# Optimization experiments

Measured on AMD Instinct MI355X. Metric: run time of the kernel, lower is better.

Reference implementation:

```python
import jax, jax.numpy as jnp
import numpy as np

N = 10000          # num_nodes
E_DIR = 160000     # directed random edges before symmetrization
B = 8              # batch
IN = 64            # input_size per node
UNITS = 64         # num_units
K = 2              # max_diffusion_step -> num_matrices = K + 1
LAMBDA_MAX = 1.5   # stand-in for eigsh largest-eigenvalue estimate


def _build_scaled_laplacian():
    # L_scaled = (2/lambda_max) * (I - D^-1/2 A D^-1/2) - I, as sparse COO
    rng = np.random.default_rng(0)
    src = rng.integers(0, N, E_DIR)
    dst = rng.integers(0, N, E_DIR)
    # symmetrize A = max(A, A^T) by duplicating edges both ways
    r = np.concatenate([src, dst])
    c = np.concatenate([dst, src])
    w = np.ones(2 * E_DIR, np.float32)
    deg = np.zeros(N, np.float32)
    np.add.at(deg, r, w)
    d_inv_sqrt = np.where(deg > 0, deg ** -0.5, 0.0).astype(np.float32)
    coef = np.float32(2.0 / LAMBDA_MAX)
    off_vals = (-coef * d_inv_sqrt[r] * d_inv_sqrt[c] * w).astype(np.float32)
    diag_idx = np.arange(N, dtype=np.int32)
    diag_vals = np.full(N, coef - 1.0, np.float32)
    rows = np.concatenate([r.astype(np.int32), diag_idx])
    cols = np.concatenate([c.astype(np.int32), diag_idx])
    vals = np.concatenate([off_vals, diag_vals])
    return rows, cols, vals  # nnz = 2*E_DIR + N = 330000


def setup_inputs() -> dict:
    key = jax.random.key(0)
    k_in, k_w = jax.random.split(key)
    rows, cols, vals = _build_scaled_laplacian()
    num_matrices = K + 1
    fan_in = IN * num_matrices
    xavier = np.sqrt(6.0 / (fan_in + UNITS)).astype(np.float32)
    return {
        "inputs": jax.random.normal(k_in, (B, N * IN), dtype=jnp.float32),
        "rows": jnp.asarray(rows),
        "cols": jnp.asarray(cols),
        "vals": jnp.asarray(vals),
        "weights": jax.random.uniform(k_w, (fan_in, UNITS), dtype=jnp.float32,
                                      minval=-xavier, maxval=xavier),
        "biases": jnp.zeros((UNITS,), dtype=jnp.float32),
    }


def reference(inputs, rows, cols, vals, weights, biases):
    batch = inputs.shape[0]
    x = inputs.reshape(batch, N, -1)              # [B, N, in]
    in_size = x.shape[2]
    # x0: [N, in*B]
    x0 = jnp.transpose(x, (1, 2, 0)).reshape(N, in_size * batch)

    def spmm(h):  # sparse Laplacian @ dense
        return jax.ops.segment_sum(vals[:, None] * h[cols], rows, num_segments=N)

    # Chebyshev recursion: T0 = x0, T1 = L x0, Tk = 2 L Tk-1 - Tk-2
    xs = [x0]
    x1 = spmm(x0)
    xs.append(x1)
    xk_1, xk_2 = x1, x0
    for _ in range(2, K + 1):
        x2 = 2.0 * spmm(xk_1) - xk_2
        xs.append(x2)
        xk_1, xk_2 = x2, xk_1

    num_matrices = K + 1
    xcat = jnp.stack(xs, axis=0)                              # [M, N, in*B]
    xcat = xcat.reshape(num_matrices, N, in_size, batch)      # [M, N, in, B]
    xcat = jnp.transpose(xcat, (3, 1, 2, 0))                  # [B, N, in, M]
    xcat = xcat.reshape(batch * N, in_size * num_matrices)
    out = xcat @ weights + biases
    return out.reshape(batch, N, UNITS)
```

## Files before the change

kernel.cpp:

```cpp
#include <hip/hip_runtime.h>
#include <hip/hip_fp16.h>

#define N_NODES 10000
#define BATCH   8
#define IN_SZ   64
#define UNITS   64
#define ROW_U   256
#define RCAP    96
#define STR     (N_NODES * 64)

typedef unsigned int uint;
typedef unsigned short ushort;
typedef __attribute__((ext_vector_type(8))) _Float16 half8;
typedef __attribute__((ext_vector_type(4))) float float4v;
typedef __attribute__((ext_vector_type(4))) uint uint4v;
typedef __attribute__((ext_vector_type(2))) uint uint2v;

__device__ inline uint f2bf_bits(float f) {
    uint u = __float_as_uint(f);
    uint r = ((u >> 16) & 1u) + 0x7FFFu;
    return (u + r) >> 16;
}
__device__ inline uint pack2h(float a, float b) {
    return (uint)__half_as_ushort(__float2half(a)) |
           ((uint)__half_as_ushort(__float2half(b)) << 16);
}
__device__ inline float h_lo(uint u) {
    return __half2float(__ushort_as_half((ushort)(u & 0xFFFFu)));
}
__device__ inline float h_hi(uint u) {
    return __half2float(__ushort_as_half((ushort)(u >> 16)));
}


__global__ __launch_bounds__(256) void k_transpose_scatter(
    const float4v* __restrict__ in4, uint* __restrict__ x0,
    const int* __restrict__ rows, const int* __restrict__ cols,
    const float* __restrict__ vals, uint* __restrict__ cursor,
    uint* __restrict__ edges, const float* __restrict__ W,
    ushort* __restrict__ wt, int nnz) {
    int gid = blockIdx.x * 256 + threadIdx.x;
    uint V = cursor[N_NODES];
    if (gid < nnz) {
        int  r   = rows[gid];
        uint pos = atomicAdd(&cursor[r], 1u) - V;
        edges[r * RCAP + pos] = (uint)cols[gid] | (f2bf_bits(vals[gid]) << 16);
    }
    if (gid < 192 * 64) {
        int u   = gid / 192;
        int col = gid - u * 192;
        int m   = col >> 6, i = col & 63;
        wt[gid] = (ushort)__half_as_ushort(__float2half(W[(i * 3 + m) * 64 + u]));
    }
    int i4 = gid & 15;
    int b  = (gid >> 4) & 7;
    int n  = gid >> 7;
    float4v v = __builtin_nontemporal_load(
        &in4[((size_t)b * N_NODES + n) * 16 + i4]);
    int c_u = b * 32 + i4 * 2;
    int q   = c_u >> 6;
    uint2v pk;
    pk.x = pack2h(v.x, v.y);
    pk.y = pack2h(v.z, v.w);
    *(uint2v*)(x0 + (size_t)q * STR + (size_t)n * 64 + (c_u & 63)) = pk;
}

#define READE(EP, KB)                                                         \
    {                                                                         \
        uint _es = ((KB) < 8) ? erec : erec2;                                 \
        int  _i0 = (((KB) * 8) & 63);                                         \
        _Pragma("unroll") for (int jj = 0; jj < 8; ++jj)                      \
            EP[jj] = __builtin_amdgcn_readlane(_es, _i0 + jj);                \
    }

#define GATHERX(XR, EP)                                                       \
    _Pragma("unroll") for (int jj = 0; jj < 8; ++jj) {                        \
        uint c = EP[jj] & 0x3FFFu;                                            \
        if (c > N_NODES - 1) c = N_NODES - 1;      \
        XR[jj] = xq[c * 64u + lane];             \
    }

#define FMA8(EP, XR)                                                          \
    _Pragma("unroll") for (int jj = 0; jj < 8; ++jj) {                        \
        float vj = __uint_as_float(EP[jj] & 0xFFFF0000u);    \
        a0 += vj * h_lo(XR[jj]);                           \
        a1 += vj * h_hi(XR[jj]);                           \
    }

__global__ __launch_bounds__(256) void k_spmm(const uint* __restrict__ cursor,
                                              const uint* __restrict__ edges,
                                              const uint* __restrict__ xin,
                                              uint* __restrict__ xout,
                                              const uint* __restrict__ xsub,
                                              float scale) {
    int L    = blockIdx.x;
    int q    = (L & 7) >> 1;
    int rb   = ((L >> 3) << 1) | (L & 1);
    int wave = threadIdx.x >> 6;
    uint lane = threadIdx.x & 63;
    int row  = rb * 4 + wave;

    const uint* xq = xin + (size_t)q * STR;
    int base = row * RCAP;
    uint V   = cursor[N_NODES];
    int cnt  = (int)__builtin_amdgcn_readfirstlane(cursor[row] - V);
    int nblk = (cnt + 7) >> 3;

    uint erec = edges[base + (int)lane];
    if ((int)lane >= cnt) erec &= 0x3FFFu;
    uint erec2 = 0;
    if (cnt > 64) {
        erec2 = edges[base + 64 + (int)lane];
        if ((int)lane + 64 >= cnt) erec2 &= 0x3FFFu;
    }

    uint sx = 0;
    if (xsub) sx = xsub[(size_t)q * STR + (size_t)row * 64 + lane];

    float a0 = 0.f, a1 = 0.f;
    uint epA[8], epB[8], xA[8], xB[8];
    READE(epA, 0);
    GATHERX(xA, epA);
    int k = 0;
    for (; k + 2 <= nblk; k += 2) {
        READE(epB, k + 1);
        GATHERX(xB, epB);
        FMA8(epA, xA);
        if (k + 2 < nblk) {
            READE(epA, k + 2);
            GATHERX(xA, epA);
        }
        FMA8(epB, xB);
    }
    if (k < nblk) FMA8(epA, xA);

    float o0 = scale * a0, o1 = scale * a1;
    if (xsub) {
        o0 -= h_lo(sx);
        o1 -= h_hi(sx);
    }
    xout[(size_t)q * STR + (size_t)row * 64 + lane] = pack2h(o0, o1);
}

__global__ __launch_bounds__(256) void k_combine(const uint* __restrict__ x0,
                                                 const uint* __restrict__ x1,
                                                 const uint* __restrict__ x2,
                                                 const ushort* __restrict__ wt,
                                                 const float* __restrict__ bias,
                                                 uint* __restrict__ cursor,
                                                 float* __restrict__ out) {
    __shared__ ushort sWt[64][200];
    int t = threadIdx.x;
    int gidc = blockIdx.x * 256 + t;
    if (gidc <= N_NODES) cursor[gidc] = 0u;
    for (int c = t; c < 1536; c += 256) {
        int row = c / 24;
        int col = (c - row * 24) * 8;
        *(uint4v*)&sWt[row][col] = *(const uint4v*)&wt[c * 8];
    }
    __syncthreads();

    int wave = t >> 6, lane = t & 63;
    int mrow = lane & 15, quad = lane >> 4;
    int L    = blockIdx.x;
    int b    = L & 7;
    int n0   = (L >> 3) * 64 + wave * 16;

    const uint* xs[3] = {x0, x1, x2};
    int an = n0 + mrow;
    if (an > N_NODES - 1) an = N_NODES - 1;

    half8 af[6];
#pragma unroll
    for (int kb = 0; kb < 6; ++kb) {
        int mat = kb >> 1;
        int c_u = b * 32 + (kb & 1) * 16 + quad * 4;
        int q   = c_u >> 6;
        af[kb] = *(const half8*)(xs[mat] + (size_t)q * STR +
                                 (size_t)an * 64 + (c_u & 63));
    }

    float4v acc[4];
#pragma unroll
    for (int ut = 0; ut < 4; ++ut) acc[ut] = (float4v){0.f, 0.f, 0.f, 0.f};

#pragma unroll
    for (int kb = 0; kb < 6; ++kb)
#pragma unroll
        for (int ut = 0; ut < 4; ++ut)
            acc[ut] = __builtin_amdgcn_mfma_f32_16x16x32_f16(
                af[kb],
                *(const half8*)&sWt[ut * 16 + mrow][kb * 32 + quad * 8],
                acc[ut], 0, 0, 0);

#pragma unroll
    for (int ut = 0; ut < 4; ++ut) {
        float bv = bias[ut * 16 + mrow];
        int u = ut * 16 + mrow;
#pragma unroll
        for (int r = 0; r < 4; ++r) {
            int n = n0 + quad * 4 + r;
            if (n < N_NODES)
                __builtin_nontemporal_store(acc[ut][r] + bv,
                    &out[((size_t)b * N_NODES + n) * UNITS + u]);
        }
    }
}

extern "C" void kernel_launch(void* const* d_in, const int* in_sizes, int n_in,
                              void* d_out, int out_size, void* d_ws, size_t ws_size,
                              hipStream_t stream) {
    const float* inputs = (const float*)d_in[0];
    const int*   rows   = (const int*)d_in[1];
    const int*   cols   = (const int*)d_in[2];
    const float* vals   = (const float*)d_in[3];
    const float* W      = (const float*)d_in[4];
    const float* bias   = (const float*)d_in[5];
    float*       out    = (float*)d_out;
    int nnz = in_sizes[1];

    char* p = (char*)d_ws;
    auto alloc = [&](size_t bytes) {
        char* r = p;
        p += (bytes + 255) & ~(size_t)255;
        return r;
    };
    uint*   x0     = (uint*)alloc(sizeof(uint) * (size_t)N_NODES * ROW_U);
    uint*   x1     = (uint*)alloc(sizeof(uint) * (size_t)N_NODES * ROW_U);
    uint*   x2     = (uint*)alloc(sizeof(uint) * (size_t)N_NODES * ROW_U);
    uint*   cursor = (uint*)alloc(sizeof(uint) * (N_NODES + 64));
    uint*   edges  = (uint*)alloc(sizeof(uint) * ((size_t)N_NODES * RCAP + 128));
    ushort* wt     = (ushort*)alloc(sizeof(ushort) * 192 * 64);

    k_transpose_scatter<<<5000, 256, 0, stream>>>(
        (const float4v*)inputs, x0, rows, cols, vals, cursor, edges, W, wt,
        nnz);
    k_spmm<<<N_NODES, 256, 0, stream>>>(cursor, edges, x0, x1, nullptr, 1.0f);
    k_spmm<<<N_NODES, 256, 0, stream>>>(cursor, edges, x1, x2, x0, 2.0f);
    k_combine<<<157 * 8, 256, 0, stream>>>(x0, x1, x2, wt, bias, cursor, out);
}
```

Measured before the change: 163.5 us.

## Fuse second Chebyshev SpMM with weight combine, keeping T2 in LDS

The second sparse multiply (2·L·x1 − x0) is merged into the MFMA combine kernel. Each 1024-thread block computes 16 rows of x2 for one batch quarter into shared memory and immediately multiplies them with the weights, so the x2 buffer is never written to or read from global memory and one launch disappears. Per-row edge counts are now saved by the first SpMM, and the cursor is reset by storing the base value V instead of zeroing. In exchange the combine stage uses only 8 of 16 waves, reads weights from global memory rather than a shared-memory copy, and depends on larger blocks.

New measurement: 177.1 us. 1.08x slower.

```diff
diff --git a/kernel.cpp b/kernel.cpp
--- a/kernel.cpp
+++ b/kernel.cpp
@@ -87,12 +87,28 @@
         a1 += vj * h_hi(XR[jj]);                           \
     }
 
+#define EDGE_PIPELINE()                                                       \
+    uint epA[8], epB[8], xA[8], xB[8];                                        \
+    READE(epA, 0);                                                            \
+    GATHERX(xA, epA);                                                         \
+    int k = 0;                                                                \
+    for (; k + 2 <= nblk; k += 2) {                                           \
+        READE(epB, k + 1);                                                    \
+        GATHERX(xB, epB);                                                     \
+        FMA8(epA, xA);                                                        \
+        if (k + 2 < nblk) {                                                   \
+            READE(epA, k + 2);                                                \
+            GATHERX(xA, epA);                                                 \
+        }                                                                     \
+        FMA8(epB, xB);                                                        \
+    }                                                                         \
+    if (k < nblk) FMA8(epA, xA);
+
 __global__ __launch_bounds__(256) void k_spmm(const uint* __restrict__ cursor,
+                                              int* __restrict__ cnts,
                                               const uint* __restrict__ edges,
                                               const uint* __restrict__ xin,
-                                              uint* __restrict__ xout,
-                                              const uint* __restrict__ xsub,
-                                              float scale) {
+                                              uint* __restrict__ xout) {
     int L    = blockIdx.x;
     int q    = (L & 7) >> 1;
     int rb   = ((L >> 3) << 1) | (L & 1);
@@ -100,10 +116,12 @@
     uint lane = threadIdx.x & 63;
     int row  = rb * 4 + wave;
 
-    const uint* xq = xin + (size_t)q * STR;
+    const uint* xq = xin;
+    xq += (size_t)q * STR;
     int base = row * RCAP;
     uint V   = cursor[N_NODES];
     int cnt  = (int)__builtin_amdgcn_readfirstlane(cursor[row] - V);
+    if (lane == 0) cnts[row] = cnt;
     int nblk = (cnt + 7) >> 3;
 
     uint erec = edges[base + (int)lane];
@@ -114,95 +132,88 @@
         if ((int)lane + 64 >= cnt) erec2 &= 0x3FFFu;
     }
 
-    uint sx = 0;
-    if (xsub) sx = xsub[(size_t)q * STR + (size_t)row * 64 + lane];
-
     float a0 = 0.f, a1 = 0.f;
-    uint epA[8], epB[8], xA[8], xB[8];
-    READE(epA, 0);
-    GATHERX(xA, epA);
-    int k = 0;
-    for (; k + 2 <= nblk; k += 2) {
-        READE(epB, k + 1);
-        GATHERX(xB, epB);
-        FMA8(epA, xA);
-        if (k + 2 < nblk) {
-            READE(epA, k + 2);
-            GATHERX(xA, epA);
-        }
-        FMA8(epB, xB);
-    }
-    if (k < nblk) FMA8(epA, xA);
-
-    float o0 = scale * a0, o1 = scale * a1;
-    if (xsub) {
-        o0 -= h_lo(sx);
-        o1 -= h_hi(sx);
-    }
-    xout[(size_t)q * STR + (size_t)row * 64 + lane] = pack2h(o0, o1);
-}
-
-__global__ __launch_bounds__(256) void k_combine(const uint* __restrict__ x0,
-                                                 const uint* __restrict__ x1,
-                                                 const uint* __restrict__ x2,
-                                                 const ushort* __restrict__ wt,
-                                                 const float* __restrict__ bias,
-                                                 uint* __restrict__ cursor,
-                                                 float* __restrict__ out) {
-    __shared__ ushort sWt[64][200];
-    int t = threadIdx.x;
-    int gidc = blockIdx.x * 256 + t;
-    if (gidc <= N_NODES) cursor[gidc] = 0u;
-    for (int c = t; c < 1536; c += 256) {
-        int row = c / 24;
-        int col = (c - row * 24) * 8;
-        *(uint4v*)&sWt[row][col] = *(const uint4v*)&wt[c * 8];
+    EDGE_PIPELINE();
+
+    xout[(size_t)q * STR + (size_t)row * 64 + lane] = pack2h(a0, a1);
+}
+
+__global__ __launch_bounds__(1024, 8) void k_spmm2_combine(
+    uint* __restrict__ cursor, const int* __restrict__ cnts,
+    const uint* __restrict__ edges,
+    const uint* __restrict__ x0, const uint* __restrict__ x1,
+    const ushort* __restrict__ wt, const float* __restrict__ bias,
+    float* __restrict__ out) {
+    __shared__ uint x2L[16][68];
+    int t    = threadIdx.x;
+    int w    = t >> 6;
+    uint lane = t & 63;
+    int L    = blockIdx.x;
+    int q    = (L & 7) >> 1;
+    int mi16 = ((L >> 3) << 1) | (L & 1);
+    if (mi16 >= 625) return;
+    int n0   = mi16 * 16;
+
+    {
+        int row  = n0 + w;
+        const uint* xq = x1 + (size_t)q * STR;
+        int base = row * RCAP;
+        uint V   = cursor[N_NODES];
+        int cnt  = __builtin_amdgcn_readfirstlane(cnts[row]);
+        if (lane == 0) cursor[row] = V;
+        int nblk = (cnt + 7) >> 3;
+
+        uint erec = edges[base + (int)lane];
+        if ((int)lane >= cnt) erec &= 0x3FFFu;
+        uint erec2 = 0;
+        if (cnt > 64) {
+            erec2 = edges[base + 64 + (int)lane];
+            if ((int)lane + 64 >= cnt) erec2 &= 0x3FFFu;
+        }
+        uint sx = x0[(size_t)q * STR + (size_t)row * 64 + lane];
+
+        float a0 = 0.f, a1 = 0.f;
+        EDGE_PIPELINE();
+        x2L[w][lane] = pack2h(2.f * a0 - h_lo(sx), 2.f * a1 - h_hi(sx));
     }
     __syncthreads();
 
-    int wave = t >> 6, lane = t & 63;
-    int mrow = lane & 15, quad = lane >> 4;
-    int L    = blockIdx.x;
-    int b    = L & 7;
-    int n0   = (L >> 3) * 64 + wave * 16;
-
-    const uint* xs[3] = {x0, x1, x2};
-    int an = n0 + mrow;
-    if (an > N_NODES - 1) an = N_NODES - 1;
-
-    half8 af[6];
-#pragma unroll
-    for (int kb = 0; kb < 6; ++kb) {
-        int mat = kb >> 1;
-        int c_u = b * 32 + (kb & 1) * 16 + quad * 4;
-        int q   = c_u >> 6;
-        af[kb] = *(const half8*)(xs[mat] + (size_t)q * STR +
-                                 (size_t)an * 64 + (c_u & 63));
-    }
-
-    float4v acc[4];
-#pragma unroll
-    for (int ut = 0; ut < 4; ++ut) acc[ut] = (float4v){0.f, 0.f, 0.f, 0.f};
-
-#pragma unroll
-    for (int kb = 0; kb < 6; ++kb)
-#pragma unroll
-        for (int ut = 0; ut < 4; ++ut)
-            acc[ut] = __builtin_amdgcn_mfma_f32_16x16x32_f16(
-                af[kb],
-                *(const half8*)&sWt[ut * 16 + mrow][kb * 32 + quad * 8],
-                acc[ut], 0, 0, 0);
-
-#pragma unroll
-    for (int ut = 0; ut < 4; ++ut) {
+    if (w < 8) {
+        int mrow = lane & 15, quad = lane >> 4;
+        int b  = 2 * q + (w >> 2);
+        int ut = w & 3;
+        int an = n0 + mrow;
+
+        const uint* xsg[2] = {x0, x1};
+        half8 af[6];
+#pragma unroll
+        for (int kb = 0; kb < 4; ++kb) {
+            int c_u = b * 32 + (kb & 1) * 16 + quad * 4;
+            af[kb] = *(const half8*)(xsg[kb >> 1] + (size_t)q * STR +
+                                     (size_t)an * 64 + (c_u & 63));
+        }
+#pragma unroll
+        for (int kb = 4; kb < 6; ++kb) {
+            int c_u = b * 32 + (kb & 1) * 16 + quad * 4;
+            af[kb] = *(const half8*)&x2L[mrow][c_u & 63];
+        }
+
+        float4v acc = (float4v){0.f, 0.f, 0.f, 0.f};
+#pragma unroll
+        for (int kb = 0; kb < 6; ++kb) {
+            half8 bf = *(const half8*)&wt[(size_t)(ut * 16 + mrow) * 192 +
+                                          kb * 32 + quad * 8];
+            acc = __builtin_amdgcn_mfma_f32_16x16x32_f16(af[kb], bf, acc,
+                                                         0, 0, 0);
+        }
+
         float bv = bias[ut * 16 + mrow];
         int u = ut * 16 + mrow;
 #pragma unroll
         for (int r = 0; r < 4; ++r) {
             int n = n0 + quad * 4 + r;
-            if (n < N_NODES)
-                __builtin_nontemporal_store(acc[ut][r] + bv,
-                    &out[((size_t)b * N_NODES + n) * UNITS + u]);
+            __builtin_nontemporal_store(acc[r] + bv,
+                &out[((size_t)b * N_NODES + n) * UNITS + u]);
         }
     }
 }
@@ -227,15 +238,15 @@
     };
     uint*   x0     = (uint*)alloc(sizeof(uint) * (size_t)N_NODES * ROW_U);
     uint*   x1     = (uint*)alloc(sizeof(uint) * (size_t)N_NODES * ROW_U);
-    uint*   x2     = (uint*)alloc(sizeof(uint) * (size_t)N_NODES * ROW_U);
     uint*   cursor = (uint*)alloc(sizeof(uint) * (N_NODES + 64));
+    int*    cnts   = (int*)alloc(sizeof(int) * (N_NODES + 64));
     uint*   edges  = (uint*)alloc(sizeof(uint) * ((size_t)N_NODES * RCAP + 128));
     ushort* wt     = (ushort*)alloc(sizeof(ushort) * 192 * 64);
 
     k_transpose_scatter<<<5000, 256, 0, stream>>>(
         (const float4v*)inputs, x0, rows, cols, vals, cursor, edges, W, wt,
         nnz);
-    k_spmm<<<N_NODES, 256, 0, stream>>>(cursor, edges, x0, x1, nullptr, 1.0f);
-    k_spmm<<<N_NODES, 256, 0, stream>>>(cursor, edges, x1, x2, x0, 2.0f);
-    k_combine<<<157 * 8, 256, 0, stream>>>(x0, x1, x2, wt, bias, cursor, out);
-}
+    k_spmm<<<N_NODES, 256, 0, stream>>>(cursor, cnts, edges, x0, x1);
+    k_spmm2_combine<<<2504, 1024, 0, stream>>>(cursor, cnts, edges, x0, x1,
+                                               wt, bias, out);
+}
```
